# Performance work log

Hardware: AMD Instinct MI355X
Metric: run time of the kernel (lower is better)

## Reference

```python
import jax, jax.numpy as jnp
import numpy as np

LIGAND_W = 1.0
SIDECHAIN_W = 0.5
LIGAND_DIST_W = 0.2
SIDECHAIN_DIST_W = 0.1
CUTOFF = 5.0
EPS = 1e-12


def _pdist(x):
    # x: [..., N, 3] -> (dist [..., N, N], sq [..., N, N]); safe sqrt for grads
    d = x[..., :, None, :] - x[..., None, :, :]
    sq = jnp.sum(d * d, axis=-1)
    return jnp.sqrt(jnp.maximum(sq, EPS)), sq


def _masked_dist_loss(pred, tgt, valid):
    # pred/tgt: [..., N, 3], valid: [..., N] float. Returns (per-group loss, has-any flag)
    pd, _ = _pdist(pred)
    td, tsq = _pdist(tgt)
    pair = valid[..., :, None] * valid[..., None, :]
    dmask = pair * (tsq > 0.0).astype(pred.dtype) * (td <= CUTOFF).astype(pred.dtype)
    num = jnp.sum(dmask * (pd - td) ** 2, axis=(-1, -2))
    den = jnp.sum(dmask, axis=(-1, -2))
    return num / jnp.maximum(den, 1.0), den > 0.0


def setup_inputs() -> dict:
    key = jax.random.key(0)
    k1, k2, k3, k4, k5, k6 = jax.random.split(key, 6)
    B, L, R, A = 64, 512, 1024, 14
    ligand_tgt = jax.random.normal(k2, (B, L, 3), dtype=jnp.float32) * 3.0
    ligand_pred = ligand_tgt + 0.5 * jax.random.normal(k1, (B, L, 3), dtype=jnp.float32)
    sidechain_tgt = jax.random.normal(k4, (B, R, A, 3), dtype=jnp.float32) * 2.0
    sidechain_pred = sidechain_tgt + 0.5 * jax.random.normal(k3, (B, R, A, 3), dtype=jnp.float32)
    ligand_mask = jax.random.bernoulli(k5, 0.9, (B, L))
    atom_mask = jax.random.bernoulli(k6, 0.7, (B, R, A))
    return {
        'ligand_pred': ligand_pred, 'ligand_tgt': ligand_tgt,
        'sidechain_pred': sidechain_pred, 'sidechain_tgt': sidechain_tgt,
        'ligand_mask': ligand_mask, 'atom_mask': atom_mask,
    }


def reference(ligand_pred, ligand_tgt, sidechain_pred, sidechain_tgt, ligand_mask, atom_mask):
    f = ligand_pred.dtype
    lm = ligand_mask.astype(f)              # [B, L]
    am = atom_mask.astype(f)                # [B, R, A]

    # --- ligand coord loss: per-batch mse (mean over valid atoms * 3), then mean over batches ---
    se = jnp.sum((ligand_pred - ligand_tgt) ** 2, axis=-1) * lm   # [B, L]
    lig_cnt = jnp.sum(lm, axis=-1)                                # [B]
    ligand_loss = jnp.mean(jnp.sum(se, axis=-1) / (3.0 * jnp.maximum(lig_cnt, 1.0)))

    # --- ligand distance-preservation loss ---
    lig_d, lig_has = _masked_dist_loss(ligand_pred, ligand_tgt, lm)  # [B], [B]
    ligand_dist_loss = jnp.sum(jnp.where(lig_has, lig_d, 0.0)) / jnp.maximum(jnp.sum(lig_has.astype(f)), 1.0)

    # --- sidechain coord loss: per-atom mse (mean over 3), mean over all valid atoms ---
    atom_mse = jnp.mean((sidechain_pred - sidechain_tgt) ** 2, axis=-1)  # [B, R, A]
    sc_cnt = jnp.sum(am)
    sidechain_loss = jnp.sum(atom_mse * am) / jnp.maximum(sc_cnt, 1.0)

    # --- sidechain distance-preservation loss: per-residue groups ---
    sc_d, sc_has = _masked_dist_loss(sidechain_pred, sidechain_tgt, am)  # [B, R]
    sidechain_dist_loss = jnp.sum(jnp.where(sc_has, sc_d, 0.0)) / jnp.maximum(jnp.sum(sc_has.astype(f)), 1.0)

    total = (LIGAND_W * ligand_loss
             + LIGAND_DIST_W * ligand_dist_loss
             + SIDECHAIN_W * sidechain_loss
             + SIDECHAIN_DIST_W * sidechain_dist_loss)
    return total
```

## Files before the change

kernel.cpp:

```cpp
#include <hip/hip_runtime.h>

#define CUTOFF 5.0f
#define DEPS 1e-12f
#define FSQRT(x) __builtin_amdgcn_sqrtf(x)


#define NSC_BLK 512
#define NLIG_BLK 512
#define GRID (NSC_BLK + NLIG_BLK)

__global__ __launch_bounds__(256) void fused_kernel(
    const float* __restrict__ lig_pred, const float* __restrict__ lig_tgt,
    const int* __restrict__ lig_mask,
    const float* __restrict__ sc_pred, const float* __restrict__ sc_tgt,
    const int* __restrict__ sc_mask,
    float* __restrict__ ws) {
  const int tid = threadIdx.x;
  __shared__ float4 stage4[1344];
  __shared__ float red[4][4];

  if (blockIdx.x < NSC_BLK) {
    float ax[7], ay[7], az[7];
    float bx[7], by[7], bz[7];
    float m[7];

    const float4* srcp = (const float4*)(sc_pred + (size_t)blockIdx.x * 5376);
    for (int k = tid; k < 1344; k += 256) stage4[k] = srcp[k];
    __syncthreads();
    {
      const float* s = ((const float*)stage4) + tid * 21;
#pragma unroll
      for (int a = 0; a < 7; a++) { ax[a] = s[3 * a]; ay[a] = s[3 * a + 1]; az[a] = s[3 * a + 2]; }
    }
    __syncthreads();
    const float4* srct = (const float4*)(sc_tgt + (size_t)blockIdx.x * 5376);
    for (int k = tid; k < 1344; k += 256) stage4[k] = srct[k];
    __syncthreads();
    {
      const float* s = ((const float*)stage4) + tid * 21;
#pragma unroll
      for (int a = 0; a < 7; a++) { bx[a] = s[3 * a]; by[a] = s[3 * a + 1]; bz[a] = s[3 * a + 2]; }
    }
    const int* mp = sc_mask + (size_t)blockIdx.x * 1792 + tid * 7;
#pragma unroll
    for (int a = 0; a < 7; a++) m[a] = (mp[a] != 0) ? 1.f : 0.f;

    float mse = 0.f, am = 0.f;
#pragma unroll
    for (int a = 0; a < 7; a++) {
      float dx = ax[a] - bx[a], dy = ay[a] - by[a], dz = az[a] - bz[a];
      mse += m[a] * ((dx * dx + dy * dy + dz * dz) * (1.f / 3.f));
      am += m[a];
    }

    float num = 0.f, den = 0.f;
#pragma unroll
    for (int js = 0; js < 7; js++) {
#pragma unroll
      for (int side = 0; side < 2; side++) {
        float jx, jy, jz, kx, ky, kz, mj;
        if (side == 0) {
          jx = ax[js]; jy = ay[js]; jz = az[js];
          kx = bx[js]; ky = by[js]; kz = bz[js];
          mj = m[js];
        } else {
          jx = __shfl_xor(ax[js], 1, 64); jy = __shfl_xor(ay[js], 1, 64);
          jz = __shfl_xor(az[js], 1, 64);
          kx = __shfl_xor(bx[js], 1, 64); ky = __shfl_xor(by[js], 1, 64);
          kz = __shfl_xor(bz[js], 1, 64);
          mj = __shfl_xor(m[js], 1, 64);
        }
#pragma unroll
        for (int i = 0; i < 7; i++) {
          float dx = bx[i] - kx, dy = by[i] - ky, dz = bz[i] - kz;
          float tsq = dx * dx + dy * dy + dz * dz;
          float td = FSQRT(fmaxf(tsq, DEPS));
          float w = m[i] * mj;
          w = (tsq > 0.f) ? w : 0.f;
          w = (td <= CUTOFF) ? w : 0.f;
          float qx = ax[i] - jx, qy = ay[i] - jy, qz = az[i] - jz;
          float pd = FSQRT(fmaxf(qx * qx + qy * qy + qz * qz, DEPS));
          float d = pd - td;
          num += w * d * d;
          den += w;
        }
      }
    }
    float num_g = num + __shfl_xor(num, 1, 64);
    float den_g = den + __shfl_xor(den, 1, 64);
    float val = (den_g > 0.f) ? 0.5f * (num_g / fmaxf(den_g, 1.f)) : 0.f;
    float has = (den_g > 0.f) ? 0.5f : 0.f;

    for (int off = 32; off > 0; off >>= 1) {
      mse += __shfl_down(mse, off, 64);
      am += __shfl_down(am, off, 64);
      val += __shfl_down(val, off, 64);
      has += __shfl_down(has, off, 64);
    }
    int lane = tid & 63, wv = tid >> 6;
    if (lane == 0) { red[0][wv] = mse; red[1][wv] = am; red[2][wv] = val; red[3][wv] = has; }
    __syncthreads();
    if (tid == 0) {
      float* p = ws + 1088 + (size_t)blockIdx.x * 4;
      p[0] = red[0][0] + red[0][1] + red[0][2] + red[0][3];
      p[1] = red[1][0] + red[1][1] + red[1][2] + red[1][3];
      p[2] = red[2][0] + red[2][1] + red[2][2] + red[2][3];
      p[3] = red[3][0] + red[3][1] + red[3][2] + red[3][3];
    }
  } else {
    const int L = 512;
    const int lb = blockIdx.x - NSC_BLK;
    const int b = lb >> 3;
    const int tile = lb & 7;
    const int i0 = tile * 64;
    const float* pb = lig_pred + (size_t)b * L * 3;
    const float* tb = lig_tgt + (size_t)b * L * 3;
    const int* mb = lig_mask + (size_t)b * L;

    float4* st4 = stage4;
    float4* sp4 = stage4 + 64;

    float pjx[2], pjy[2], pjz[2], tjx[2], tjy[2], tjz[2], mj[2];
#pragma unroll
    for (int k = 0; k < 2; k++) {
      int j = k * 256 + tid;
      pjx[k] = pb[3 * j]; pjy[k] = pb[3 * j + 1]; pjz[k] = pb[3 * j + 2];
      tjx[k] = tb[3 * j]; tjy[k] = tb[3 * j + 1]; tjz[k] = tb[3 * j + 2];
      mj[k] = (mb[j] != 0) ? 1.f : 0.f;
    }
    if (tid < 64) {
      int i = i0 + tid;
      st4[tid] = make_float4(tb[3 * i], tb[3 * i + 1], tb[3 * i + 2], (mb[i] != 0) ? 1.f : 0.f);
    } else if (tid < 128) {
      int i = i0 + tid - 64;
      sp4[tid - 64] = make_float4(pb[3 * i], pb[3 * i + 1], pb[3 * i + 2], 0.f);
    }
    __syncthreads();

    float se = 0.f, cnt = 0.f;
    if (tile == 0) {
#pragma unroll
      for (int k = 0; k < 2; k++) {
        float dx = pjx[k] - tjx[k], dy = pjy[k] - tjy[k], dz = pjz[k] - tjz[k];
        se += mj[k] * (dx * dx + dy * dy + dz * dz);
        cnt += mj[k];
      }
    }

    float num = 0.f, den = 0.f;
#pragma unroll 4
    for (int ii = 0; ii < 64; ii++) {
      float4 ti = st4[ii];
      float4 pi = sp4[ii];
#pragma unroll
      for (int k = 0; k < 2; k++) {
        float w = ti.w * mj[k];
        float dx = ti.x - tjx[k], dy = ti.y - tjy[k], dz = ti.z - tjz[k];
        float tsq = dx * dx + dy * dy + dz * dz;
        float td = FSQRT(fmaxf(tsq, DEPS));
        w = (tsq > 0.f) ? w : 0.f;
        w = (td <= CUTOFF) ? w : 0.f;
        float qx = pi.x - pjx[k], qy = pi.y - pjy[k], qz = pi.z - pjz[k];
        float pd = FSQRT(fmaxf(qx * qx + qy * qy + qz * qz, DEPS));
        float d = pd - td;
        num += w * d * d;
        den += w;
      }
    }

    for (int off = 32; off > 0; off >>= 1) {
      num += __shfl_down(num, off, 64);
      den += __shfl_down(den, off, 64);
      se += __shfl_down(se, off, 64);
      cnt += __shfl_down(cnt, off, 64);
    }
    int lane = tid & 63, wv = tid >> 6;
    if (lane == 0) { red[0][wv] = num; red[1][wv] = den; red[2][wv] = se; red[3][wv] = cnt; }
    __syncthreads();
    if (tid == 0) {
      ws[lb * 2 + 0] = red[0][0] + red[0][1] + red[0][2] + red[0][3];
      ws[lb * 2 + 1] = red[1][0] + red[1][1] + red[1][2] + red[1][3];
      if (tile == 0) {
        float se_t = red[2][0] + red[2][1] + red[2][2] + red[2][3];
        float cnt_t = red[3][0] + red[3][1] + red[3][2] + red[3][3];
        ws[1024 + b] = se_t / (3.f * fmaxf(cnt_t, 1.f));
      }
    }
  }
}

__global__ __launch_bounds__(256) void finalize_kernel(const float* __restrict__ ws,
                                                       float* __restrict__ out) {
  const int tid = threadIdx.x;
  __shared__ float sred[4][4];

  const float* sc = ws + 1088;
  float s0 = 0.f, s1 = 0.f, s2 = 0.f, s3 = 0.f;
  for (int i = tid; i < 512; i += 256) {
    s0 += sc[4 * i + 0]; s1 += sc[4 * i + 1]; s2 += sc[4 * i + 2]; s3 += sc[4 * i + 3];
  }
  for (int off = 32; off > 0; off >>= 1) {
    s0 += __shfl_down(s0, off, 64);
    s1 += __shfl_down(s1, off, 64);
    s2 += __shfl_down(s2, off, 64);
    s3 += __shfl_down(s3, off, 64);
  }
  int lane = tid & 63, wv = tid >> 6;
  if (lane == 0) { sred[0][wv] = s0; sred[1][wv] = s1; sred[2][wv] = s2; sred[3][wv] = s3; }
  __syncthreads();

  float lval = 0.f, lhas = 0.f, lcoord = 0.f;
  if (tid < 64) {
    float n = 0.f, d = 0.f;
    for (int t = 0; t < 8; t++) {
      n += ws[(tid * 8 + t) * 2 + 0];
      d += ws[(tid * 8 + t) * 2 + 1];
    }
    lval = (d > 0.f) ? n / fmaxf(d, 1.f) : 0.f;
    lhas = (d > 0.f) ? 1.f : 0.f;
    lcoord = ws[1024 + tid];
    for (int off = 32; off > 0; off >>= 1) {
      lval += __shfl_down(lval, off, 64);
      lhas += __shfl_down(lhas, off, 64);
      lcoord += __shfl_down(lcoord, off, 64);
    }
  }
  if (tid == 0) {
    float sc_mse = sred[0][0] + sred[0][1] + sred[0][2] + sred[0][3];
    float sc_am = sred[1][0] + sred[1][1] + sred[1][2] + sred[1][3];
    float sc_val = sred[2][0] + sred[2][1] + sred[2][2] + sred[2][3];
    float sc_has = sred[3][0] + sred[3][1] + sred[3][2] + sred[3][3];
    float ligand_loss = lcoord * (1.f / 64.f);
    float ligand_dist_loss = lval / fmaxf(lhas, 1.f);
    float sidechain_loss = sc_mse / fmaxf(sc_am, 1.f);
    float sidechain_dist_loss = sc_val / fmaxf(sc_has, 1.f);
    out[0] = ligand_loss + 0.2f * ligand_dist_loss + 0.5f * sidechain_loss +
             0.1f * sidechain_dist_loss;
  }
}

extern "C" void kernel_launch(void* const* d_in, const int* in_sizes, int n_in,
                              void* d_out, int out_size, void* d_ws, size_t ws_size,
                              hipStream_t stream) {
  const float* ligand_pred = (const float*)d_in[0];
  const float* ligand_tgt = (const float*)d_in[1];
  const float* sidechain_pred = (const float*)d_in[2];
  const float* sidechain_tgt = (const float*)d_in[3];
  const int* ligand_mask = (const int*)d_in[4];
  const int* atom_mask = (const int*)d_in[5];
  float* out = (float*)d_out;
  float* ws = (float*)d_ws;

  fused_kernel<<<GRID, 256, 0, stream>>>(ligand_pred, ligand_tgt, ligand_mask,
                                         sidechain_pred, sidechain_tgt, atom_mask, ws);
  finalize_kernel<<<1, 256, 0, stream>>>(ws, out);
}
```

Measured before the change: 106.7 us.

## Exploit pair symmetry in ligand distance loss and interleave block types

The ligand distance loss now evaluates only pairs with j > i. Each tile's threads take j from the tile start to the end of the ligand, instead of every j against every i. Because the loss is num/den and both sums are halved together, the ratio is unchanged, and the diagonal is already masked by tsq > 0. Sidechain and ligand blocks now alternate by block index parity so the two workloads mix across the GPU. The cost is uneven per-tile work, since later tiles have far fewer active threads, plus branch divergence from the js < L guard.

```diff
diff --git a/kernel.cpp b/kernel.cpp
--- a/kernel.cpp
+++ b/kernel.cpp
@@ -5,9 +5,7 @@
 #define FSQRT(x) __builtin_amdgcn_sqrtf(x)
 
 
-#define NSC_BLK 512
-#define NLIG_BLK 512
-#define GRID (NSC_BLK + NLIG_BLK)
+#define GRID 1024
 
 __global__ __launch_bounds__(256) void fused_kernel(
     const float* __restrict__ lig_pred, const float* __restrict__ lig_tgt,
@@ -19,12 +17,13 @@
   __shared__ float4 stage4[1344];
   __shared__ float red[4][4];
 
-  if (blockIdx.x < NSC_BLK) {
+  if ((blockIdx.x & 1) == 0) {
+    const int sb = blockIdx.x >> 1;
     float ax[7], ay[7], az[7];
     float bx[7], by[7], bz[7];
     float m[7];
 
-    const float4* srcp = (const float4*)(sc_pred + (size_t)blockIdx.x * 5376);
+    const float4* srcp = (const float4*)(sc_pred + (size_t)sb * 5376);
     for (int k = tid; k < 1344; k += 256) stage4[k] = srcp[k];
     __syncthreads();
     {
@@ -33,7 +32,7 @@
       for (int a = 0; a < 7; a++) { ax[a] = s[3 * a]; ay[a] = s[3 * a + 1]; az[a] = s[3 * a + 2]; }
     }
     __syncthreads();
-    const float4* srct = (const float4*)(sc_tgt + (size_t)blockIdx.x * 5376);
+    const float4* srct = (const float4*)(sc_tgt + (size_t)sb * 5376);
     for (int k = tid; k < 1344; k += 256) stage4[k] = srct[k];
     __syncthreads();
     {
@@ -41,7 +40,7 @@
 #pragma unroll
       for (int a = 0; a < 7; a++) { bx[a] = s[3 * a]; by[a] = s[3 * a + 1]; bz[a] = s[3 * a + 2]; }
     }
-    const int* mp = sc_mask + (size_t)blockIdx.x * 1792 + tid * 7;
+    const int* mp = sc_mask + (size_t)sb * 1792 + tid * 7;
 #pragma unroll
     for (int a = 0; a < 7; a++) m[a] = (mp[a] != 0) ? 1.f : 0.f;
 
@@ -101,7 +100,7 @@
     if (lane == 0) { red[0][wv] = mse; red[1][wv] = am; red[2][wv] = val; red[3][wv] = has; }
     __syncthreads();
     if (tid == 0) {
-      float* p = ws + 1088 + (size_t)blockIdx.x * 4;
+      float* p = ws + 1088 + (size_t)sb * 4;
       p[0] = red[0][0] + red[0][1] + red[0][2] + red[0][3];
       p[1] = red[1][0] + red[1][1] + red[1][2] + red[1][3];
       p[2] = red[2][0] + red[2][1] + red[2][2] + red[2][3];
@@ -109,7 +108,7 @@
     }
   } else {
     const int L = 512;
-    const int lb = blockIdx.x - NSC_BLK;
+    const int lb = blockIdx.x >> 1;
     const int b = lb >> 3;
     const int tile = lb & 7;
     const int i0 = tile * 64;
@@ -120,14 +119,6 @@
     float4* st4 = stage4;
     float4* sp4 = stage4 + 64;
 
-    float pjx[2], pjy[2], pjz[2], tjx[2], tjy[2], tjz[2], mj[2];
-#pragma unroll
-    for (int k = 0; k < 2; k++) {
-      int j = k * 256 + tid;
-      pjx[k] = pb[3 * j]; pjy[k] = pb[3 * j + 1]; pjz[k] = pb[3 * j + 2];
-      tjx[k] = tb[3 * j]; tjy[k] = tb[3 * j + 1]; tjz[k] = tb[3 * j + 2];
-      mj[k] = (mb[j] != 0) ? 1.f : 0.f;
-    }
     if (tid < 64) {
       int i = i0 + tid;
       st4[tid] = make_float4(tb[3 * i], tb[3 * i + 1], tb[3 * i + 2], (mb[i] != 0) ? 1.f : 0.f);
@@ -137,34 +128,35 @@
     }
     __syncthreads();
 
-    float se = 0.f, cnt = 0.f;
-    if (tile == 0) {
-#pragma unroll
-      for (int k = 0; k < 2; k++) {
-        float dx = pjx[k] - tjx[k], dy = pjy[k] - tjy[k], dz = pjz[k] - tjz[k];
-        se += mj[k] * (dx * dx + dy * dy + dz * dz);
-        cnt += mj[k];
-      }
-    }
-
-    float num = 0.f, den = 0.f;
+    float num = 0.f, den = 0.f, se = 0.f, cnt = 0.f;
+#pragma unroll
+    for (int k = 0; k < 2; k++) {
+      const int js = i0 + k * 256 + tid;
+      if (js < L) {
+        float pjx = pb[3 * js], pjy = pb[3 * js + 1], pjz = pb[3 * js + 2];
+        float tjx = tb[3 * js], tjy = tb[3 * js + 1], tjz = tb[3 * js + 2];
+        float mj = (mb[js] != 0) ? 1.f : 0.f;
+        if (tile == 0) {
+          float dx = pjx - tjx, dy = pjy - tjy, dz = pjz - tjz;
+          se += mj * (dx * dx + dy * dy + dz * dz);
+          cnt += mj;
+        }
 #pragma unroll 4
-    for (int ii = 0; ii < 64; ii++) {
-      float4 ti = st4[ii];
-      float4 pi = sp4[ii];
-#pragma unroll
-      for (int k = 0; k < 2; k++) {
-        float w = ti.w * mj[k];
-        float dx = ti.x - tjx[k], dy = ti.y - tjy[k], dz = ti.z - tjz[k];
-        float tsq = dx * dx + dy * dy + dz * dz;
-        float td = FSQRT(fmaxf(tsq, DEPS));
-        w = (tsq > 0.f) ? w : 0.f;
-        w = (td <= CUTOFF) ? w : 0.f;
-        float qx = pi.x - pjx[k], qy = pi.y - pjy[k], qz = pi.z - pjz[k];
-        float pd = FSQRT(fmaxf(qx * qx + qy * qy + qz * qz, DEPS));
-        float d = pd - td;
-        num += w * d * d;
-        den += w;
+        for (int ii = 0; ii < 64; ii++) {
+          float4 ti = st4[ii];
+          float4 pi = sp4[ii];
+          float w = (js > i0 + ii) ? ti.w * mj : 0.f;
+          float dx = ti.x - tjx, dy = ti.y - tjy, dz = ti.z - tjz;
+          float tsq = dx * dx + dy * dy + dz * dz;
+          float td = FSQRT(fmaxf(tsq, DEPS));
+          w = (tsq > 0.f) ? w : 0.f;
+          w = (td <= CUTOFF) ? w : 0.f;
+          float qx = pi.x - pjx, qy = pi.y - pjy, qz = pi.z - pjz;
+          float pd = FSQRT(fmaxf(qx * qx + qy * qy + qz * qz, DEPS));
+          float d = pd - td;
+          num += w * d * d;
+          den += w;
+        }
       }
     }
 
```

Result: slower. 109.9 us (+2.9%).
